# Optimization experiments

Hardware: AMD Instinct MI355X
Metric: run time of the kernel (lower is better)

Reference implementation:

```python
import jax, jax.numpy as jnp
import numpy as np

NUM_GROUPS = 32
EPS = 1e-6


def group_norm(x, gamma, beta):
    b, c, h, w = x.shape
    xg = x.reshape(b, NUM_GROUPS, c // NUM_GROUPS, h, w)
    mean = jnp.mean(xg, axis=(2, 3, 4), keepdims=True)
    var = jnp.var(xg, axis=(2, 3, 4), keepdims=True)
    xg = (xg - mean) * jax.lax.rsqrt(var + EPS)
    x = xg.reshape(b, c, h, w)
    return x * gamma[None, :, None, None] + beta[None, :, None, None]


def conv1x1(x, w, b):
    # x: [B,C,H,W], w: [Cout,Cin], b: [Cout]
    return jnp.einsum('bchw,oc->bohw', x, w) + b[None, :, None, None]


def setup_inputs() -> dict:
    key = jax.random.key(0)
    ks = jax.random.split(key, 11)
    B, C, H, W = 2, 512, 64, 64
    s = 1.0 / np.sqrt(C)
    return {
        'x': jax.random.normal(ks[0], (B, C, H, W), jnp.float32),
        'norm_gamma': jnp.ones((C,), jnp.float32),
        'norm_beta': jnp.zeros((C,), jnp.float32),
        'wq': jax.random.normal(ks[1], (C, C), jnp.float32) * s,
        'bq': jnp.zeros((C,), jnp.float32),
        'wk': jax.random.normal(ks[2], (C, C), jnp.float32) * s,
        'bk': jnp.zeros((C,), jnp.float32),
        'wv': jax.random.normal(ks[3], (C, C), jnp.float32) * s,
        'bv': jnp.zeros((C,), jnp.float32),
        'wo': jax.random.normal(ks[4], (C, C), jnp.float32) * s,
        'bo': jnp.zeros((C,), jnp.float32),
    }


def reference(x, norm_gamma, norm_beta, wq, bq, wk, bk, wv, bv, wo, bo):
    b, c, h, w = x.shape
    hn = group_norm(x, norm_gamma, norm_beta)
    q = conv1x1(hn, wq, bq).reshape(b, c, h * w)  # [B,C,HW]
    k = conv1x1(hn, wk, bk).reshape(b, c, h * w)
    v = conv1x1(hn, wv, bv).reshape(b, c, h * w)
    scale = jnp.asarray(c, x.dtype) ** -0.5
    # scores[b,i,j] = sum_c q[b,c,i] * k[b,c,j]
    scores = jnp.einsum('bci,bcj->bij', q, k) * scale
    attn = jax.nn.softmax(scores, axis=2)
    # out[b,c,i] = sum_j v[b,c,j] * attn[b,i,j]
    out = jnp.einsum('bcj,bij->bci', v, attn).reshape(b, c, h, w)
    out = conv1x1(out, wo, bo)
    return x + out
```

## Files before the change

### kernel.cpp

```cpp
#include <hip/hip_runtime.h>
#include <hip/hip_bf16.h>

using u16 = unsigned short;
typedef __attribute__((ext_vector_type(4))) float f32x4;
typedef __attribute__((ext_vector_type(8))) __bf16 bf16x8;
typedef __attribute__((ext_vector_type(8))) short s16x8;
typedef __attribute__((ext_vector_type(4))) short s16x4;

#define DEVI __device__ __forceinline__

constexpr int BATCH = 2, C = 512, HW = 4096, NG = 32, CPG = 16;

DEVI float b2f(u16 u) { union { unsigned u; float f; } a; a.u = ((unsigned)u) << 16; return a.f; }
DEVI u16 f2b(float f) {
  union { float f; unsigned u; } a; a.f = f;
  unsigned r = a.u + 0x7fffu + ((a.u >> 16) & 1u);
  return (u16)(r >> 16);
}

__global__ __launch_bounds__(256) void cvt_w(const float* __restrict__ a, const float* __restrict__ b,
                                             const float* __restrict__ c, const float* __restrict__ d,
                                             u16* __restrict__ out) {
  int i = blockIdx.x * 256 + threadIdx.x;
  int w = i >> 16;
  int off = (i & 65535) * 4;
  const float* s = (w == 0) ? a : (w == 1) ? b : (w == 2) ? c : d;
  f32x4 v = *(const f32x4*)(s + off);
  s16x4 o;
  o[0] = (short)f2b(v[0]); o[1] = (short)f2b(v[1]); o[2] = (short)f2b(v[2]); o[3] = (short)f2b(v[3]);
  *(s16x4*)(out + (size_t)w * 262144 + off) = o;
}

__global__ __launch_bounds__(1024) void gn_stats(const float* __restrict__ x, float* __restrict__ stats) {
  int bg = blockIdx.x;
  const f32x4* xg = (const f32x4*)(x + (size_t)bg * (CPG * HW));
  float s = 0.f, ss = 0.f;
  for (int i = threadIdx.x; i < CPG * HW / 4; i += 1024) {
    f32x4 v = xg[i];
    s += v[0] + v[1] + v[2] + v[3];
    ss += v[0] * v[0] + v[1] * v[1] + v[2] * v[2] + v[3] * v[3];
  }
  #pragma unroll
  for (int o = 32; o; o >>= 1) { s += __shfl_xor(s, o); ss += __shfl_xor(ss, o); }
  __shared__ float red[32];
  int wv = threadIdx.x >> 6, ln = threadIdx.x & 63;
  if (ln == 0) { red[wv] = s; red[16 + wv] = ss; }
  __syncthreads();
  if (threadIdx.x == 0) {
    float S = 0.f, SS = 0.f;
    for (int i = 0; i < 16; ++i) { S += red[i]; SS += red[16 + i]; }
    float inv = 1.f / (float)(CPG * HW);
    float mean = S * inv;
    float var = SS * inv - mean * mean;
    stats[bg * 2] = mean;
    stats[bg * 2 + 1] = rsqrtf(var + 1e-6f);
  }
}

__global__ __launch_bounds__(256) void gn_normT(const float* __restrict__ x, const float* __restrict__ stats,
                                                const float* __restrict__ gamma, const float* __restrict__ beta,
                                                u16* __restrict__ hnT) {
  __shared__ u16 tile[64][66];
  int b = blockIdx.z, c0 = blockIdx.y * 64, h0 = blockIdx.x * 64;
  int t = threadIdx.x;
  const float* xb = x + ((size_t)b * C + c0) * HW + h0;
  int r = t / 16, cc = (t % 16) * 4;
  #pragma unroll
  for (int it = 0; it < 4; ++it) {
    int rr = it * 16 + r;
    int ch = c0 + rr;
    int g = b * NG + (ch >> 4);
    float mean = stats[g * 2], rstd = stats[g * 2 + 1];
    float ga = gamma[ch] * rstd;
    float be = beta[ch] - mean * ga;
    f32x4 v = *(const f32x4*)(xb + (size_t)rr * HW + cc);
    #pragma unroll
    for (int j = 0; j < 4; ++j) tile[rr][cc + j] = f2b(v[j] * ga + be);
  }
  __syncthreads();
  u16* op = hnT + (size_t)b * HW * C + (size_t)h0 * C + c0;
  int hr2 = t / 8, cg = (t % 8) * 8;
  #pragma unroll
  for (int it = 0; it < 2; ++it) {
    int hr = it * 32 + hr2;
    s16x8 o8;
    #pragma unroll
    for (int j = 0; j < 8; ++j) o8[j] = (short)tile[cg + j][hr];
    *(s16x8*)(op + (size_t)hr * C + cg) = o8;
  }
}

#define EPI_BIAS_M 1
#define EPI_BIAS_N 2
#define EPI_RESID  4
#define EPI_F32OUT 8
#define EPI_SCALE  16

template <int EPI>
__global__ __launch_bounds__(256) void gemm_bt(const u16* __restrict__ A, const u16* __restrict__ Bt,
                                               void* __restrict__ Co, int M, int N, int K,
                                               long long sA, long long sB, long long sC,
                                               const float* __restrict__ bias,
                                               const float* __restrict__ resid, long long sR, float scale) {
  (void)M;
  __shared__ u16 ldsA[128 * 64];
  __shared__ u16 ldsB[128 * 64];
  const int tid = threadIdx.x;
  const int bz = blockIdx.z;
  const int bm = blockIdx.y, bn = blockIdx.x;
  A += (size_t)bz * sA;
  Bt += (size_t)bz * sB;
  const int wave = tid >> 6, lane = tid & 63;
  const int wr = wave >> 1, wc = wave & 1;
  f32x4 acc[4][4] = {};

  const int srow = tid >> 3;
  const int sch = (tid & 7) ^ (srow & 7);
  const u16* gA = A + (size_t)(bm * 128 + srow) * K + sch * 8;
  const u16* gB = Bt + (size_t)(bn * 128 + srow) * K + sch * 8;
  u16* lA = ldsA + wave * 512;
  u16* lB = ldsB + wave * 512;

  for (int k0 = 0; k0 < K; k0 += 64) {
    #pragma unroll
    for (int cc = 0; cc < 4; ++cc) {
      __builtin_amdgcn_global_load_lds(
          (const __attribute__((address_space(1))) void*)(gA + (size_t)cc * 32 * K + k0),
          (__attribute__((address_space(3))) void*)(lA + cc * 2048), 16, 0, 0);
      __builtin_amdgcn_global_load_lds(
          (const __attribute__((address_space(1))) void*)(gB + (size_t)cc * 32 * K + k0),
          (__attribute__((address_space(3))) void*)(lB + cc * 2048), 16, 0, 0);
    }
    __syncthreads();
    #pragma unroll
    for (int kk = 0; kk < 2; ++kk) {
      bf16x8 af[4], bfv[4];
      #pragma unroll
      for (int m = 0; m < 4; ++m) {
        int r = wr * 64 + m * 16 + (lane & 15);
        int chunk = (kk * 4 + (lane >> 4)) ^ (r & 7);
        af[m] = *(const bf16x8*)(ldsA + r * 64 + chunk * 8);
      }
      #pragma unroll
      for (int n = 0; n < 4; ++n) {
        int r = wc * 64 + n * 16 + (lane & 15);
        int chunk = (kk * 4 + (lane >> 4)) ^ (r & 7);
        bfv[n] = *(const bf16x8*)(ldsB + r * 64 + chunk * 8);
      }
      #pragma unroll
      for (int m = 0; m < 4; ++m)
        #pragma unroll
        for (int n = 0; n < 4; ++n)
          acc[m][n] = __builtin_amdgcn_mfma_f32_16x16x32_bf16(af[m], bfv[n], acc[m][n], 0, 0, 0);
    }
    __syncthreads();
  }

  const int col0 = bn * 128 + wc * 64;
  const int row0 = bm * 128 + wr * 64 + ((lane >> 4) << 2);
  #pragma unroll
  for (int m = 0; m < 4; ++m) {
    #pragma unroll
    for (int j = 0; j < 4; ++j) {
      int gm = row0 + m * 16 + j;
      float bm_v = (EPI & EPI_BIAS_M) ? bias[gm] : 0.f;
      #pragma unroll
      for (int n = 0; n < 4; ++n) {
        int gn = col0 + n * 16 + (lane & 15);
        float v = acc[m][n][j];
        if (EPI & EPI_SCALE) v *= scale;
        v += bm_v;
        if (EPI & EPI_BIAS_N) v += bias[gn];
        if (EPI & EPI_RESID) v += resid[(size_t)bz * sR + (size_t)gm * N + gn];
        if (EPI & EPI_F32OUT)
          ((float*)Co)[(size_t)bz * sC + (size_t)gm * N + gn] = v;
        else
          ((u16*)Co)[(size_t)bz * sC + (size_t)gm * N + gn] = f2b(v);
      }
    }
  }
}

__global__ __launch_bounds__(256) void softmax_rows(u16* __restrict__ S) {
  int row = blockIdx.x * 4 + (threadIdx.x >> 6);
  int lane = threadIdx.x & 63;
  s16x8* p = (s16x8*)(S + (size_t)row * 4096);
  float v[64];
  float m = -1e30f;
  #pragma unroll
  for (int j = 0; j < 8; ++j) {
    s16x8 raw = p[j * 64 + lane];
    #pragma unroll
    for (int e = 0; e < 8; ++e) {
      float f = b2f((u16)raw[e]);
      v[j * 8 + e] = f;
      m = fmaxf(m, f);
    }
  }
  #pragma unroll
  for (int o = 32; o; o >>= 1) m = fmaxf(m, __shfl_xor(m, o));
  float s = 0.f;
  #pragma unroll
  for (int i = 0; i < 64; ++i) { v[i] = __expf(v[i] - m); s += v[i]; }
  #pragma unroll
  for (int o = 32; o; o >>= 1) s += __shfl_xor(s, o);
  float r = 1.f / s;
  #pragma unroll
  for (int j = 0; j < 8; ++j) {
    s16x8 o8;
    #pragma unroll
    for (int e = 0; e < 8; ++e) o8[e] = (short)f2b(v[j * 8 + e] * r);
    p[j * 64 + lane] = o8;
  }
}

extern "C" void kernel_launch(void* const* d_in, const int* in_sizes, int n_in,
                              void* d_out, int out_size, void* d_ws, size_t ws_size,
                              hipStream_t stream) {
  (void)in_sizes; (void)n_in; (void)out_size; (void)ws_size;
  const float* x     = (const float*)d_in[0];
  const float* gamma = (const float*)d_in[1];
  const float* beta  = (const float*)d_in[2];
  const float* wq    = (const float*)d_in[3];
  const float* bq    = (const float*)d_in[4];
  const float* wk    = (const float*)d_in[5];
  const float* bk    = (const float*)d_in[6];
  const float* wv    = (const float*)d_in[7];
  const float* bv    = (const float*)d_in[8];
  const float* wo    = (const float*)d_in[9];
  const float* bo    = (const float*)d_in[10];

  char* ws = (char*)d_ws;
  const size_t NTOK = (size_t)HW * C;
  float* stats = (float*)ws;
  u16* wbf = (u16*)(ws + 1024);
  size_t off = 1024 + (size_t)4 * 262144 * 2;
  u16* hnT = (u16*)(ws + off); off += (size_t)BATCH * NTOK * 2;
  u16* qT  = (u16*)(ws + off); off += (size_t)BATCH * NTOK * 2;
  u16* kT  = (u16*)(ws + off); off += (size_t)BATCH * NTOK * 2;
  u16* vv  = (u16*)(ws + off); off += (size_t)BATCH * NTOK * 2;
  u16* aoT = (u16*)(ws + off); off += (size_t)BATCH * NTOK * 2;
  u16* Sm  = (u16*)(ws + off);

  const long long sTok = (long long)HW * C;
  const long long sS   = (long long)HW * HW;
  const float scale = 0.044194173824159216f;

  cvt_w<<<dim3(1024), dim3(256), 0, stream>>>(wq, wk, wv, wo, wbf);
  gn_stats<<<dim3(64), dim3(1024), 0, stream>>>(x, stats);
  gn_normT<<<dim3(HW / 64, C / 64, BATCH), dim3(256), 0, stream>>>(x, stats, gamma, beta, hnT);

  gemm_bt<EPI_BIAS_N><<<dim3(4, 32, BATCH), dim3(256), 0, stream>>>(
      hnT, wbf + 0 * 262144, qT, HW, C, C, sTok, 0, sTok, bq, nullptr, 0, 0.f);
  gemm_bt<EPI_BIAS_N><<<dim3(4, 32, BATCH), dim3(256), 0, stream>>>(
      hnT, wbf + 1 * 262144, kT, HW, C, C, sTok, 0, sTok, bk, nullptr, 0, 0.f);
  gemm_bt<EPI_BIAS_M><<<dim3(32, 4, BATCH), dim3(256), 0, stream>>>(
      wbf + 2 * 262144, hnT, vv, C, HW, C, 0, sTok, sTok, bv, nullptr, 0, 0.f);
  gemm_bt<EPI_SCALE><<<dim3(32, 32, BATCH), dim3(256), 0, stream>>>(
      qT, kT, Sm, HW, HW, C, sTok, sTok, sS, nullptr, nullptr, 0, scale);
  softmax_rows<<<dim3(2048), dim3(256), 0, stream>>>(Sm);
  gemm_bt<0><<<dim3(4, 32, BATCH), dim3(256), 0, stream>>>(
      Sm, vv, aoT, HW, C, HW, sS, sTok, sTok, nullptr, nullptr, 0, 0.f);
  gemm_bt<EPI_BIAS_M | EPI_RESID | EPI_F32OUT><<<dim3(32, 4, BATCH), dim3(256), 0, stream>>>(
      wbf + 3 * 262144, aoT, d_out, C, HW, C, 0, sTok, (long long)C * HW, bo, x, (long long)C * HW, 0.f);
}
```

Before: 221.5 us.

## Use 256x256 pipelined GEMM for QK^T and split-K PV with reduction

Adds a 512-thread 256x256-tile GEMM kernel that double-buffers operands in LDS through direct global-to-LDS loads, interleaving fragment loads with MFMA. It replaces the QK^T score GEMM and the PV GEMM. The PV GEMM is now split four ways along K to raise parallelism, with a separate kernel summing the bf16 partials. Workspace is re-laid out so buffers alias: the partials overwrite hnT/qT/kT and spill into d_out. This adds an extra reduction pass and rounds partials to bf16 before summing, which could cost some accuracy.

```diff
diff --git a/kernel.cpp b/kernel.cpp
--- a/kernel.cpp
+++ b/kernel.cpp
@@ -94,14 +94,13 @@
 #define EPI_BIAS_N 2
 #define EPI_RESID  4
 #define EPI_F32OUT 8
-#define EPI_SCALE  16
 
 template <int EPI>
 __global__ __launch_bounds__(256) void gemm_bt(const u16* __restrict__ A, const u16* __restrict__ Bt,
                                                void* __restrict__ Co, int M, int N, int K,
                                                long long sA, long long sB, long long sC,
                                                const float* __restrict__ bias,
-                                               const float* __restrict__ resid, long long sR, float scale) {
+                                               const float* __restrict__ resid, long long sR) {
   (void)M;
   __shared__ u16 ldsA[128 * 64];
   __shared__ u16 ldsB[128 * 64];
@@ -167,9 +166,7 @@
       #pragma unroll
       for (int n = 0; n < 4; ++n) {
         int gn = col0 + n * 16 + (lane & 15);
-        float v = acc[m][n][j];
-        if (EPI & EPI_SCALE) v *= scale;
-        v += bm_v;
+        float v = acc[m][n][j] + bm_v;
         if (EPI & EPI_BIAS_N) v += bias[gn];
         if (EPI & EPI_RESID) v += resid[(size_t)bz * sR + (size_t)gm * N + gn];
         if (EPI & EPI_F32OUT)
@@ -181,6 +178,123 @@
   }
 }
 
+template <bool SCALED>
+__global__ __launch_bounds__(512, 2) void gemm256(
+    const u16* __restrict__ Ag, const u16* __restrict__ Bg,
+    u16* __restrict__ Co, u16* __restrict__ Co2, int zSwitch,
+    int Nld, int ldK, int nsplitLog, int kLen,
+    long long sA, long long sB, long long sC, float scale) {
+  __shared__ u16 lds[65536];
+  const int tid = threadIdx.x;
+  const int lane = tid & 63, w = tid >> 6;
+  const int wm = w >> 2, wn = w & 3;
+  const int l15 = lane & 15, l4 = lane >> 4;
+  const int bn = blockIdx.x, bm = blockIdx.y;
+  const int z = blockIdx.z;
+  const int bz = z >> nsplitLog, kz = z & ((1 << nsplitLog) - 1);
+  const int kStart = kz * kLen;
+  const int NT = kLen >> 6;
+
+  const int rStage = w * 8 + (lane >> 3);
+  const int gch = (lane & 7) ^ (lane >> 3);
+  const u16* gA = Ag + (size_t)bz * sA + (size_t)(bm * 256) * ldK + kStart + gch * 8;
+  const u16* gB = Bg + (size_t)bz * sB + (size_t)(bn * 256) * ldK + kStart + gch * 8;
+
+  f32x4 acc[8][4] = {};
+  bf16x8 aF[4][2], bF[2][2][2];
+
+  const int hB = wn >> 1, qB = wn & 1;
+  const u16* pA0 = lds + (0 * 4 + wm) * 8192;
+  const u16* pA1 = lds + (1 * 4 + wm) * 8192;
+  const u16* pB0 = lds + (0 * 4 + 2 + hB) * 8192;
+  const u16* pB1 = lds + (1 * 4 + 2 + hB) * 8192;
+
+  #define STAGE(TT, DB, AB, HF) { \
+    const u16* gbase = (AB) ? gB : gA; \
+    u16* l0 = lds + ((DB) * 4 + (AB) * 2 + (HF)) * 8192 + w * 512; \
+    _Pragma("unroll") for (int s = 0; s < 2; ++s) { \
+      const u16* gp = gbase + (size_t)((HF) * 128 + s * 64 + rStage) * ldK + (TT) * 64; \
+      __builtin_amdgcn_global_load_lds((const __attribute__((address_space(1))) void*)gp, \
+          (__attribute__((address_space(3))) void*)(l0 + s * 4096), 16, 0, 0); } }
+
+  #define LOAD_A(P, MH) { _Pragma("unroll") for (int j = 0; j < 4; ++j) \
+    _Pragma("unroll") for (int kk = 0; kk < 2; ++kk) { \
+      const int r_ = (MH) * 64 + j * 16 + l15; const int c_ = (kk * 4 + l4) ^ (r_ & 7); \
+      aF[j][kk] = *(const bf16x8*)((P) + r_ * 64 + c_ * 8); } }
+
+  #define LOAD_B(P, NH) { _Pragma("unroll") for (int j = 0; j < 2; ++j) \
+    _Pragma("unroll") for (int kk = 0; kk < 2; ++kk) { \
+      const int r_ = qB * 64 + (NH) * 32 + j * 16 + l15; const int c_ = (kk * 4 + l4) ^ (r_ & 7); \
+      bF[NH][j][kk] = *(const bf16x8*)((P) + r_ * 64 + c_ * 8); } }
+
+  #define MM(MH, NH) { __builtin_amdgcn_s_setprio(1); \
+    _Pragma("unroll") for (int j = 0; j < 4; ++j) \
+      _Pragma("unroll") for (int j2 = 0; j2 < 2; ++j2) \
+        _Pragma("unroll") for (int kk = 0; kk < 2; ++kk) \
+          acc[(MH) * 4 + j][(NH) * 2 + j2] = __builtin_amdgcn_mfma_f32_16x16x32_bf16( \
+              aF[j][kk], bF[NH][j2][kk], acc[(MH) * 4 + j][(NH) * 2 + j2], 0, 0, 0); \
+    __builtin_amdgcn_s_setprio(0); }
+
+  #define BAR __builtin_amdgcn_s_barrier()
+  #define WLG { asm volatile("s_waitcnt lgkmcnt(0)" ::: "memory"); __builtin_amdgcn_sched_barrier(0); }
+  #define WV4 asm volatile("s_waitcnt vmcnt(4)" ::: "memory")
+  #define WV0 asm volatile("s_waitcnt vmcnt(0)" ::: "memory")
+
+  STAGE(0, 0, 1, 0); STAGE(0, 0, 1, 1);
+  STAGE(0, 0, 0, 0); STAGE(0, 0, 0, 1);
+  STAGE(1, 1, 1, 0); STAGE(1, 1, 1, 1);
+  WV4; BAR;
+
+  const int NI = NT / 2 - 1;
+  for (int i = 0; i < NI; ++i) {
+    const int t1 = 2 * i + 1, u0 = 2 * i + 2, u1 = 2 * i + 3;
+    LOAD_A(pA0, 0); LOAD_B(pB0, 0); STAGE(t1, 1, 0, 0); BAR; WLG; MM(0, 0); BAR;
+    LOAD_B(pB0, 1); STAGE(t1, 1, 0, 1); BAR; WLG; MM(0, 1); BAR;
+    LOAD_A(pA0, 1); STAGE(u0, 0, 1, 0); BAR; WLG; MM(1, 1); BAR;
+    STAGE(u0, 0, 1, 1); BAR; WLG; MM(1, 0); WV4; BAR;
+    LOAD_A(pA1, 0); LOAD_B(pB1, 0); STAGE(u0, 0, 0, 0); BAR; WLG; MM(0, 0); BAR;
+    LOAD_B(pB1, 1); STAGE(u0, 0, 0, 1); BAR; WLG; MM(0, 1); BAR;
+    LOAD_A(pA1, 1); STAGE(u1, 1, 1, 0); BAR; WLG; MM(1, 1); BAR;
+    STAGE(u1, 1, 1, 1); BAR; WLG; MM(1, 0); WV4; BAR;
+  }
+  {
+    const int t1 = NT - 1;
+    LOAD_A(pA0, 0); LOAD_B(pB0, 0); STAGE(t1, 1, 0, 0); BAR; WLG; MM(0, 0); BAR;
+    LOAD_B(pB0, 1); STAGE(t1, 1, 0, 1); BAR; WLG; MM(0, 1); BAR;
+    LOAD_A(pA0, 1); BAR; WLG; MM(1, 1); BAR;
+    BAR; WLG; MM(1, 0); WV0; BAR;
+    LOAD_A(pA1, 0); LOAD_B(pB1, 0); BAR; WLG; MM(0, 0); BAR;
+    LOAD_B(pB1, 1); BAR; WLG; MM(0, 1); BAR;
+    LOAD_A(pA1, 1); BAR; WLG; MM(1, 1); BAR;
+    MM(1, 0);
+  }
+  #undef STAGE
+  #undef LOAD_A
+  #undef LOAD_B
+  #undef MM
+  #undef BAR
+  #undef WLG
+  #undef WV4
+  #undef WV0
+
+  u16* outp = (z < zSwitch) ? (Co + (size_t)z * sC) : (Co2 + (size_t)(z - zSwitch) * sC);
+  const int gm0 = bm * 256 + wm * 128 + l4 * 4;
+  const int gn0 = bn * 256 + wn * 64 + l15;
+  #pragma unroll
+  for (int m = 0; m < 8; ++m) {
+    #pragma unroll
+    for (int j = 0; j < 4; ++j) {
+      const size_t rowoff = (size_t)(gm0 + m * 16 + j) * Nld;
+      #pragma unroll
+      for (int n = 0; n < 4; ++n) {
+        float v = acc[m][n][j];
+        if (SCALED) v *= scale;
+        outp[rowoff + gn0 + n * 16] = f2b(v);
+      }
+    }
+  }
+}
+
 __global__ __launch_bounds__(256) void softmax_rows(u16* __restrict__ S) {
   int row = blockIdx.x * 4 + (threadIdx.x >> 6);
   int lane = threadIdx.x & 63;
@@ -212,6 +326,26 @@
     for (int e = 0; e < 8; ++e) o8[e] = (short)f2b(v[j * 8 + e] * r);
     p[j * 64 + lane] = o8;
   }
+}
+
+__global__ __launch_bounds__(256) void reduce_pv(const u16* __restrict__ P, const u16* __restrict__ P2,
+                                                 u16* __restrict__ ao) {
+  const size_t e = ((size_t)blockIdx.x * 256 + threadIdx.x) * 8;
+  const int b = (int)(e >> 21);
+  const size_t o = e & 2097151;
+  float s[8] = {0.f, 0.f, 0.f, 0.f, 0.f, 0.f, 0.f, 0.f};
+  #pragma unroll
+  for (int kz = 0; kz < 4; ++kz) {
+    const int zz = b * 4 + kz;
+    const u16* src = (zz < 6) ? (P + (size_t)zz * 2097152) : (P2 + (size_t)(zz - 6) * 2097152);
+    s16x8 v = *(const s16x8*)(src + o);
+    #pragma unroll
+    for (int j = 0; j < 8; ++j) s[j] += b2f((u16)v[j]);
+  }
+  s16x8 o8;
+  #pragma unroll
+  for (int j = 0; j < 8; ++j) o8[j] = (short)f2b(s[j]);
+  *(s16x8*)(ao + e) = o8;
 }
 
 extern "C" void kernel_launch(void* const* d_in, const int* in_sizes, int n_in,
@@ -231,16 +365,16 @@
   const float* bo    = (const float*)d_in[10];
 
   char* ws = (char*)d_ws;
-  const size_t NTOK = (size_t)HW * C;
+  const size_t MiB = 1024 * 1024;
   float* stats = (float*)ws;
   u16* wbf = (u16*)(ws + 1024);
-  size_t off = 1024 + (size_t)4 * 262144 * 2;
-  u16* hnT = (u16*)(ws + off); off += (size_t)BATCH * NTOK * 2;
-  u16* qT  = (u16*)(ws + off); off += (size_t)BATCH * NTOK * 2;
-  u16* kT  = (u16*)(ws + off); off += (size_t)BATCH * NTOK * 2;
-  u16* vv  = (u16*)(ws + off); off += (size_t)BATCH * NTOK * 2;
-  u16* aoT = (u16*)(ws + off); off += (size_t)BATCH * NTOK * 2;
-  u16* Sm  = (u16*)(ws + off);
+  u16* vv  = (u16*)(ws + 4 * MiB);
+  u16* hnT = (u16*)(ws + 12 * MiB);
+  u16* qT  = (u16*)(ws + 20 * MiB);
+  u16* kT  = (u16*)(ws + 28 * MiB);
+  u16* Ppart = (u16*)(ws + 12 * MiB);
+  u16* Sm  = (u16*)(ws + 36 * MiB);
+  u16* aoT = (u16*)(ws + 36 * MiB);
 
   const long long sTok = (long long)HW * C;
   const long long sS   = (long long)HW * HW;
@@ -251,16 +385,22 @@
   gn_normT<<<dim3(HW / 64, C / 64, BATCH), dim3(256), 0, stream>>>(x, stats, gamma, beta, hnT);
 
   gemm_bt<EPI_BIAS_N><<<dim3(4, 32, BATCH), dim3(256), 0, stream>>>(
-      hnT, wbf + 0 * 262144, qT, HW, C, C, sTok, 0, sTok, bq, nullptr, 0, 0.f);
+      hnT, wbf + 0 * 262144, qT, HW, C, C, sTok, 0, sTok, bq, nullptr, 0);
   gemm_bt<EPI_BIAS_N><<<dim3(4, 32, BATCH), dim3(256), 0, stream>>>(
-      hnT, wbf + 1 * 262144, kT, HW, C, C, sTok, 0, sTok, bk, nullptr, 0, 0.f);
+      hnT, wbf + 1 * 262144, kT, HW, C, C, sTok, 0, sTok, bk, nullptr, 0);
   gemm_bt<EPI_BIAS_M><<<dim3(32, 4, BATCH), dim3(256), 0, stream>>>(
-      wbf + 2 * 262144, hnT, vv, C, HW, C, 0, sTok, sTok, bv, nullptr, 0, 0.f);
-  gemm_bt<EPI_SCALE><<<dim3(32, 32, BATCH), dim3(256), 0, stream>>>(
-      qT, kT, Sm, HW, HW, C, sTok, sTok, sS, nullptr, nullptr, 0, scale);
+      wbf + 2 * 262144, hnT, vv, C, HW, C, 0, sTok, sTok, bv, nullptr, 0);
+
+  gemm256<true><<<dim3(16, 16, BATCH), dim3(512), 0, stream>>>(
+      qT, kT, Sm, Sm, 1000, HW, C, 0, C, sTok, sTok, sS, scale);
+
   softmax_rows<<<dim3(2048), dim3(256), 0, stream>>>(Sm);
-  gemm_bt<0><<<dim3(4, 32, BATCH), dim3(256), 0, stream>>>(
-      Sm, vv, aoT, HW, C, HW, sS, sTok, sTok, nullptr, nullptr, 0, 0.f);
+
+  gemm256<false><<<dim3(2, 16, BATCH * 4), dim3(512), 0, stream>>>(
+      Sm, vv, Ppart, (u16*)d_out, 6, C, HW, 2, HW / 4, sS, sTok, (long long)2097152, 1.f);
+
+  reduce_pv<<<dim3(2048), dim3(256), 0, stream>>>(Ppart, (const u16*)d_out, aoT);
+
   gemm_bt<EPI_BIAS_M | EPI_RESID | EPI_F32OUT><<<dim3(32, 4, BATCH), dim3(256), 0, stream>>>(
-      wbf + 3 * 262144, aoT, d_out, C, HW, C, 0, sTok, (long long)C * HW, bo, x, (long long)C * HW, 0.f);
-}
+      wbf + 3 * 262144, aoT, d_out, C, HW, C, 0, sTok, (long long)C * HW, bo, x, (long long)C * HW);
+}
```

Measured after the change: 190.7 us. -13.9%, faster.
